# Kernel optimization log

Measured on AMD Instinct MI355X. Metric: run time of the kernel, lower is better.

Reference implementation:

```python
import jax, jax.numpy as jnp
import numpy as np

H_GRID, W_GRID = 32, 32
KH, KW = 7, 11
NUM_HEADS = 8


def local_window_mask(H, W, kh, kw):
    # Token (h,w) may attend to (h',w') iff |h-h'|<=kh//2 and |w-w'|<=kw//2
    # (equivalent to the padded/cropped construction in the torch module).
    hh = jnp.arange(H)
    ww = jnp.arange(W)
    ok_h = jnp.abs(hh[:, None] - hh[None, :]) <= kh // 2  # [H,H]
    ok_w = jnp.abs(ww[:, None] - ww[None, :]) <= kw // 2  # [W,W]
    ok = ok_h[:, None, :, None] & ok_w[None, :, None, :]  # [H,W,H,W]
    ok = ok.reshape(H * W, H * W)
    return jnp.where(ok, 0.0, -jnp.inf)[None, None]  # [1,1,N,N]


def setup_inputs() -> dict:
    key = jax.random.key(0)
    k1, k2, k3, k4, k5 = jax.random.split(key, 5)
    B, N, E = 8, H_GRID * W_GRID, 256
    return {
        "x": jax.random.normal(k1, (B, N, E), dtype=jnp.float32),
        "qkv_w": jax.random.normal(k2, (3 * E, E), dtype=jnp.float32) * 0.02,
        "qkv_b": jax.random.normal(k3, (3 * E,), dtype=jnp.float32) * 0.02,
        "proj_w": jax.random.normal(k4, (E, E), dtype=jnp.float32) * 0.02,
        "proj_b": jax.random.normal(k5, (E,), dtype=jnp.float32) * 0.02,
    }


def reference(x, qkv_w, qkv_b, proj_w, proj_b):
    B, N, E = x.shape
    dh = E // NUM_HEADS
    scale = E ** (-0.5)  # note: embed_dim scaling, as in the original module
    qkv = x @ qkv_w.T + qkv_b                       # [B,N,3E]
    qkv = qkv.reshape(B, N, 3, NUM_HEADS, dh).transpose(2, 0, 3, 1, 4)
    q, k, v = qkv[0] * scale, qkv[1], qkv[2]        # [B,H,N,dh]
    attn = jnp.einsum('bhnd,bhmd->bhnm', q, k)      # [B,H,N,N]
    attn = attn + local_window_mask(H_GRID, W_GRID, KH, KW)
    attn = jax.nn.softmax(attn, axis=-1)
    out = jnp.einsum('bhnm,bhmd->bhnd', attn, v)    # [B,H,N,dh]
    out = out.transpose(0, 2, 1, 3).reshape(B, N, E)
    return out @ proj_w.T + proj_b
```

## Files before the change

kernel.cpp:

```cpp
#include <hip/hip_runtime.h>
#include <math.h>

constexpr int Bb = 8;
constexpr int Ns = 1024;
constexpr int Es = 256;
constexpr int NH = 8;
constexpr int DH = 32;
constexpr int Mrows = Bb * Ns;
constexpr int NX = Mrows * Es;
constexpr int NP = Es * Es;

typedef __bf16 bf16x8 __attribute__((ext_vector_type(8)));
typedef float  f32x4  __attribute__((ext_vector_type(4)));
union U4B8 { uint4 u; bf16x8 b; unsigned short s[8]; };

__device__ __forceinline__ unsigned short f2bf(float f) {
    union { float f; unsigned u; } c; c.f = f;
    unsigned r = (c.u + 0x7FFFu + ((c.u >> 16) & 1u)) >> 16;
    return (unsigned short)r;
}
__device__ __forceinline__ float bf2f(unsigned short h) {
    union { unsigned u; float f; } c; c.u = ((unsigned)h) << 16;
    return c.f;
}

#define GLD 72
#define PST 232

__global__ __launch_bounds__(256, 4)
void qkv_gemm(const float* __restrict__ x, const float* __restrict__ qkv_w,
              const float* __restrict__ qkv_b, const float* __restrict__ proj_w,
              unsigned short* __restrict__ qo, unsigned short* __restrict__ ko,
              unsigned short* __restrict__ vto, unsigned short* __restrict__ pwb)
{
    __shared__ unsigned short As[64 * GLD];
    __shared__ unsigned short Ws[64 * GLD];

    const int t = threadIdx.x;

    if (blockIdx.x >= 1536) {
        int i = ((int)(blockIdx.x - 1536) * 256 + t) * 4;
        float4 f = *(const float4*)(proj_w + i);
        ushort4 u;
        u.x = f2bf(f.x); u.y = f2bf(f.y); u.z = f2bf(f.z); u.w = f2bf(f.w);
        *(ushort4*)(pwb + i) = u;
        return;
    }

    const int m0 = (blockIdx.x & 127) * 64;
    const int j0 = (blockIdx.x >> 7) * 64;

    const int srow = t >> 2;
    const int scol = (t & 3) * 16;

    const int lane = t & 63;
    const int wave = t >> 6;
    const int wm = (wave & 1) * 32;
    const int wn = (wave >> 1) * 32;
    const int fm = lane & 15;
    const int fq = lane >> 4;

    f32x4 acc[2][2];
    #pragma unroll
    for (int i = 0; i < 2; i++)
        #pragma unroll
        for (int j = 0; j < 2; j++)
            acc[i][j] = (f32x4){0.f, 0.f, 0.f, 0.f};

    const float* Arow = x + (size_t)(m0 + srow) * Es;
    const float* Wrow = qkv_w + (size_t)(j0 + srow) * Es;

    for (int k0 = 0; k0 < Es; k0 += 64) {
        float4 av[4], wv[4];
        #pragma unroll
        for (int i = 0; i < 4; i++) {
            av[i] = *(const float4*)(Arow + k0 + scol + 4 * i);
            wv[i] = *(const float4*)(Wrow + k0 + scol + 4 * i);
        }
        U4B8 pa0, pa1, pw0, pw1;
        #pragma unroll
        for (int i = 0; i < 2; i++) {
            pa0.s[4*i+0] = f2bf(av[i].x);   pa0.s[4*i+1] = f2bf(av[i].y);
            pa0.s[4*i+2] = f2bf(av[i].z);   pa0.s[4*i+3] = f2bf(av[i].w);
            pa1.s[4*i+0] = f2bf(av[i+2].x); pa1.s[4*i+1] = f2bf(av[i+2].y);
            pa1.s[4*i+2] = f2bf(av[i+2].z); pa1.s[4*i+3] = f2bf(av[i+2].w);
            pw0.s[4*i+0] = f2bf(wv[i].x);   pw0.s[4*i+1] = f2bf(wv[i].y);
            pw0.s[4*i+2] = f2bf(wv[i].z);   pw0.s[4*i+3] = f2bf(wv[i].w);
            pw1.s[4*i+0] = f2bf(wv[i+2].x); pw1.s[4*i+1] = f2bf(wv[i+2].y);
            pw1.s[4*i+2] = f2bf(wv[i+2].z); pw1.s[4*i+3] = f2bf(wv[i+2].w);
        }
        __syncthreads();
        *(uint4*)&As[srow * GLD + scol]     = pa0.u;
        *(uint4*)&As[srow * GLD + scol + 8] = pa1.u;
        *(uint4*)&Ws[srow * GLD + scol]     = pw0.u;
        *(uint4*)&Ws[srow * GLD + scol + 8] = pw1.u;
        __syncthreads();
        #pragma unroll
        for (int ks = 0; ks < 64; ks += 32) {
            U4B8 af0, af1, bf0, bf1;
            af0.u = *(const uint4*)&As[(wm +      fm) * GLD + ks + fq * 8];
            af1.u = *(const uint4*)&As[(wm + 16 + fm) * GLD + ks + fq * 8];
            bf0.u = *(const uint4*)&Ws[(wn +      fm) * GLD + ks + fq * 8];
            bf1.u = *(const uint4*)&Ws[(wn + 16 + fm) * GLD + ks + fq * 8];
            acc[0][0] = __builtin_amdgcn_mfma_f32_16x16x32_bf16(af0.b, bf0.b, acc[0][0], 0, 0, 0);
            acc[0][1] = __builtin_amdgcn_mfma_f32_16x16x32_bf16(af0.b, bf1.b, acc[0][1], 0, 0, 0);
            acc[1][0] = __builtin_amdgcn_mfma_f32_16x16x32_bf16(af1.b, bf0.b, acc[1][0], 0, 0, 0);
            acc[1][1] = __builtin_amdgcn_mfma_f32_16x16x32_bf16(af1.b, bf1.b, acc[1][1], 0, 0, 0);
        }
    }

    #pragma unroll
    for (int mt = 0; mt < 2; mt++) {
        #pragma unroll
        for (int nt = 0; nt < 2; nt++) {
            #pragma unroll
            for (int r = 0; r < 4; r++) {
                int row = m0 + wm + mt * 16 + fq * 4 + r;
                int col = j0 + wn + nt * 16 + fm;
                float val = acc[mt][nt][r] + qkv_b[col];
                int part = col >> 8;
                int head = (col >> 5) & 7;
                int d = col & 31;
                int b = row >> 10;
                int n = row & 1023;
                int bh = b * NH + head;
                if (part == 0)
                    qo[((size_t)bh * Ns + n) * DH + d] = f2bf(val * 0.0625f);
                else if (part == 1)
                    ko[((size_t)bh * Ns + n) * DH + d] = f2bf(val);
                else
                    vto[((size_t)bh * DH + d) * Ns + n] = f2bf(val);
            }
        }
    }
}

__global__ __launch_bounds__(256)
void attn_mfma2(const unsigned short* __restrict__ qb, const unsigned short* __restrict__ kb,
                const unsigned short* __restrict__ vtb, unsigned short* __restrict__ aob)
{
    __shared__ unsigned short Pb[32 * PST];
    __shared__ float pmax[2][32];
    __shared__ float psum[2][32];

    const int blk = blockIdx.x;
    const int hq  = blk & 31;
    const int bh  = blk >> 5;
    const int t   = threadIdx.x;
    const int lane = t & 63;
    const int w    = t >> 6;
    const int fm = lane & 15;
    const int fq = lane >> 4;

    int n0c = (hq - 3) * 32;
    n0c = n0c < 0 ? 0 : (n0c > Ns - 224 ? Ns - 224 : n0c);

    const int qbase = (w & 1) * 16;
    const int sel   = w >> 1;
    const int dbase = (w >> 1) * 16;

    const unsigned short* vrow = vtb + ((size_t)bh * DH + dbase + fm) * Ns;
    uint4 vpre[7];
    #pragma unroll
    for (int i = 0; i < 7; i++)
        vpre[i] = *(const uint4*)(vrow + n0c + i * 32 + fq * 8);

    U4B8 qa;
    qa.u = *(const uint4*)(qb + ((size_t)bh * Ns + hq * 32 + qbase + fm) * DH + fq * 8);

    f32x4 sv[7];
    #pragma unroll
    for (int i = 0; i < 7; i++) {
        int kt = sel + 2 * i;
        U4B8 kf;
        kf.u = *(const uint4*)(kb + ((size_t)bh * Ns + n0c + kt * 16 + fm) * DH + fq * 8);
        sv[i] = __builtin_amdgcn_mfma_f32_16x16x32_bf16(qa.b, kf.b, (f32x4){0.f,0.f,0.f,0.f}, 0, 0, 0);
    }

    float mx[4] = {-INFINITY, -INFINITY, -INFINITY, -INFINITY};
    #pragma unroll
    for (int i = 0; i < 7; i++) {
        int g = n0c + (sel + 2 * i) * 16 + fm;
        int gh = g >> 5, gw = g & 31;
        int dhh = gh - hq;
        bool okh = (dhh >= -3) && (dhh <= 3);
        #pragma unroll
        for (int r = 0; r < 4; r++) {
            int qc = qbase + fq * 4 + r;
            int dww = gw - qc;
            bool ok = okh && (dww >= -5) && (dww <= 5);
            float s = ok ? sv[i][r] : -INFINITY;
            sv[i][r] = s;
            mx[r] = fmaxf(mx[r], s);
        }
    }
    #pragma unroll
    for (int r = 0; r < 4; r++)
        #pragma unroll
        for (int m = 1; m < 16; m <<= 1)
            mx[r] = fmaxf(mx[r], __shfl_xor(mx[r], m));
    if (fm == 0) {
        #pragma unroll
        for (int r = 0; r < 4; r++)
            pmax[sel][qbase + fq * 4 + r] = mx[r];
    }
    __syncthreads();

    float M[4];
    #pragma unroll
    for (int r = 0; r < 4; r++) {
        int qc = qbase + fq * 4 + r;
        M[r] = fmaxf(pmax[0][qc], pmax[1][qc]);
    }

    float sm[4] = {0.f, 0.f, 0.f, 0.f};
    #pragma unroll
    for (int i = 0; i < 7; i++) {
        int kt = sel + 2 * i;
        #pragma unroll
        for (int r = 0; r < 4; r++) {
            float p = __expf(sv[i][r] - M[r]);
            unsigned short pu = f2bf(p);
            Pb[(qbase + fq * 4 + r) * PST + kt * 16 + fm] = pu;
            sm[r] += bf2f(pu);
        }
    }
    #pragma unroll
    for (int r = 0; r < 4; r++)
        #pragma unroll
        for (int m = 1; m < 16; m <<= 1)
            sm[r] += __shfl_xor(sm[r], m);
    if (fm == 0) {
        #pragma unroll
        for (int r = 0; r < 4; r++)
            psum[sel][qbase + fq * 4 + r] = sm[r];
    }
    __syncthreads();

    f32x4 acc = (f32x4){0.f, 0.f, 0.f, 0.f};
    #pragma unroll
    for (int i = 0; i < 7; i++) {
        U4B8 pa, vb;
        pa.u = *(const uint4*)&Pb[(qbase + fm) * PST + i * 32 + fq * 8];
        vb.u = vpre[i];
        acc = __builtin_amdgcn_mfma_f32_16x16x32_bf16(pa.b, vb.b, acc, 0, 0, 0);
    }

    const int b = bh >> 3, h = bh & 7;
    #pragma unroll
    for (int r = 0; r < 4; r++) {
        int qq = qbase + fq * 4 + r;
        float inv = 1.f / (psum[0][qq] + psum[1][qq]);
        aob[((size_t)(b * Ns) + hq * 32 + qq) * Es + h * DH + dbase + fm] = f2bf(acc[r] * inv);
    }
}

__global__ __launch_bounds__(256, 4)
void proj_gemm(const unsigned short* __restrict__ A, const unsigned short* __restrict__ Wb,
               const float* __restrict__ bias, float* __restrict__ out)
{
    __shared__ unsigned short As[64 * GLD];
    __shared__ unsigned short Ws[64 * GLD];

    const int t = threadIdx.x;
    const int m0 = (blockIdx.x & 127) * 64;
    const int j0 = (blockIdx.x >> 7) * 64;

    const int srow = t >> 2;
    const int scol = (t & 3) * 16;

    const int lane = t & 63;
    const int wave = t >> 6;
    const int wm = (wave & 1) * 32;
    const int wn = (wave >> 1) * 32;
    const int fm = lane & 15;
    const int fq = lane >> 4;

    f32x4 acc[2][2];
    #pragma unroll
    for (int i = 0; i < 2; i++)
        #pragma unroll
        for (int j = 0; j < 2; j++)
            acc[i][j] = (f32x4){0.f, 0.f, 0.f, 0.f};

    const unsigned short* Arow = A + (size_t)(m0 + srow) * Es;
    const unsigned short* Wrow = Wb + (size_t)(j0 + srow) * Es;

    for (int k0 = 0; k0 < Es; k0 += 64) {
        uint4 a0 = *(const uint4*)(Arow + k0 + scol);
        uint4 a1 = *(const uint4*)(Arow + k0 + scol + 8);
        uint4 w0 = *(const uint4*)(Wrow + k0 + scol);
        uint4 w1 = *(const uint4*)(Wrow + k0 + scol + 8);
        __syncthreads();
        *(uint4*)&As[srow * GLD + scol]     = a0;
        *(uint4*)&As[srow * GLD + scol + 8] = a1;
        *(uint4*)&Ws[srow * GLD + scol]     = w0;
        *(uint4*)&Ws[srow * GLD + scol + 8] = w1;
        __syncthreads();
        #pragma unroll
        for (int ks = 0; ks < 64; ks += 32) {
            U4B8 af0, af1, bf0, bf1;
            af0.u = *(const uint4*)&As[(wm +      fm) * GLD + ks + fq * 8];
            af1.u = *(const uint4*)&As[(wm + 16 + fm) * GLD + ks + fq * 8];
            bf0.u = *(const uint4*)&Ws[(wn +      fm) * GLD + ks + fq * 8];
            bf1.u = *(const uint4*)&Ws[(wn + 16 + fm) * GLD + ks + fq * 8];
            acc[0][0] = __builtin_amdgcn_mfma_f32_16x16x32_bf16(af0.b, bf0.b, acc[0][0], 0, 0, 0);
            acc[0][1] = __builtin_amdgcn_mfma_f32_16x16x32_bf16(af0.b, bf1.b, acc[0][1], 0, 0, 0);
            acc[1][0] = __builtin_amdgcn_mfma_f32_16x16x32_bf16(af1.b, bf0.b, acc[1][0], 0, 0, 0);
            acc[1][1] = __builtin_amdgcn_mfma_f32_16x16x32_bf16(af1.b, bf1.b, acc[1][1], 0, 0, 0);
        }
    }

    #pragma unroll
    for (int mt = 0; mt < 2; mt++) {
        #pragma unroll
        for (int nt = 0; nt < 2; nt++) {
            #pragma unroll
            for (int r = 0; r < 4; r++) {
                int row = m0 + wm + mt * 16 + fq * 4 + r;
                int col = j0 + wn + nt * 16 + fm;
                out[(size_t)row * Es + col] = acc[mt][nt][r] + bias[col];
            }
        }
    }
}

extern "C" void kernel_launch(void* const* d_in, const int* in_sizes, int n_in,
                              void* d_out, int out_size, void* d_ws, size_t ws_size,
                              hipStream_t stream) {
    const float* x      = (const float*)d_in[0];
    const float* qkv_w  = (const float*)d_in[1];
    const float* qkv_b  = (const float*)d_in[2];
    const float* proj_w = (const float*)d_in[3];
    const float* proj_b = (const float*)d_in[4];
    float* out = (float*)d_out;

    unsigned short* qb  = (unsigned short*)d_ws;
    unsigned short* kb  = qb + NX;
    unsigned short* vtb = kb + NX;
    unsigned short* pwb = vtb + NX;
    unsigned short* aob = pwb + NP;

    qkv_gemm<<<dim3(1600), dim3(256), 0, stream>>>(
        x, qkv_w, qkv_b, proj_w, qb, kb, vtb, pwb);

    attn_mfma2<<<dim3(Bb * NH * 32), dim3(256), 0, stream>>>(qb, kb, vtb, aob);

    proj_gemm<<<dim3(Mrows / 64 * (Es / 64)), dim3(256), 0, stream>>>(
        aob, pwb, proj_b, out);
}
```

Before: 104.9 us.

## Pre-cast inputs and weights to bf16 in a separate kernel; remap attention block order

Adds a cast kernel that converts x, qkv_w and proj_w to bf16 once, so the QKV GEMM loads bf16 tiles directly instead of reloading fp32 and converting in every block (x was re-read by 12 column blocks). It also reorders the attention block index so the batch varies fastest, changing which (b,h,q-tile) blocks run concurrently and how they hit cache. The cost is an extra kernel launch and an extra write and read of a bf16 copy of x.

```diff
diff --git a/kernel.cpp b/kernel.cpp
--- a/kernel.cpp
+++ b/kernel.cpp
@@ -8,6 +8,7 @@
 constexpr int DH = 32;
 constexpr int Mrows = Bb * Ns;
 constexpr int NX = Mrows * Es;
+constexpr int NQ = 3 * Es * Es;
 constexpr int NP = Es * Es;
 
 typedef __bf16 bf16x8 __attribute__((ext_vector_type(8)));
@@ -27,26 +28,34 @@
 #define GLD 72
 #define PST 232
 
+__global__ __launch_bounds__(256)
+void cast_all(const float* __restrict__ x, const float* __restrict__ wq,
+              const float* __restrict__ wp, unsigned short* __restrict__ xb,
+              unsigned short* __restrict__ wqb, unsigned short* __restrict__ wpb)
+{
+    int i = (blockIdx.x * 256 + threadIdx.x) * 8;
+    const float* src; unsigned short* dst;
+    if (i < NX)            { src = x  + i;             dst = xb  + i; }
+    else if (i < NX + NQ)  { src = wq + (i - NX);      dst = wqb + (i - NX); }
+    else                   { src = wp + (i - NX - NQ); dst = wpb + (i - NX - NQ); }
+    float4 f0 = *(const float4*)src;
+    float4 f1 = *(const float4*)(src + 4);
+    U4B8 u;
+    u.s[0] = f2bf(f0.x); u.s[1] = f2bf(f0.y); u.s[2] = f2bf(f0.z); u.s[3] = f2bf(f0.w);
+    u.s[4] = f2bf(f1.x); u.s[5] = f2bf(f1.y); u.s[6] = f2bf(f1.z); u.s[7] = f2bf(f1.w);
+    *(uint4*)dst = u.u;
+}
+
 __global__ __launch_bounds__(256, 4)
-void qkv_gemm(const float* __restrict__ x, const float* __restrict__ qkv_w,
-              const float* __restrict__ qkv_b, const float* __restrict__ proj_w,
+void qkv_gemm(const unsigned short* __restrict__ A, const unsigned short* __restrict__ W,
+              const float* __restrict__ qkv_b,
               unsigned short* __restrict__ qo, unsigned short* __restrict__ ko,
-              unsigned short* __restrict__ vto, unsigned short* __restrict__ pwb)
+              unsigned short* __restrict__ vto)
 {
     __shared__ unsigned short As[64 * GLD];
     __shared__ unsigned short Ws[64 * GLD];
 
     const int t = threadIdx.x;
-
-    if (blockIdx.x >= 1536) {
-        int i = ((int)(blockIdx.x - 1536) * 256 + t) * 4;
-        float4 f = *(const float4*)(proj_w + i);
-        ushort4 u;
-        u.x = f2bf(f.x); u.y = f2bf(f.y); u.z = f2bf(f.z); u.w = f2bf(f.w);
-        *(ushort4*)(pwb + i) = u;
-        return;
-    }
-
     const int m0 = (blockIdx.x & 127) * 64;
     const int j0 = (blockIdx.x >> 7) * 64;
 
@@ -67,33 +76,19 @@
         for (int j = 0; j < 2; j++)
             acc[i][j] = (f32x4){0.f, 0.f, 0.f, 0.f};
 
-    const float* Arow = x + (size_t)(m0 + srow) * Es;
-    const float* Wrow = qkv_w + (size_t)(j0 + srow) * Es;
+    const unsigned short* Arow = A + (size_t)(m0 + srow) * Es;
+    const unsigned short* Wrow = W + (size_t)(j0 + srow) * Es;
 
     for (int k0 = 0; k0 < Es; k0 += 64) {
-        float4 av[4], wv[4];
-        #pragma unroll
-        for (int i = 0; i < 4; i++) {
-            av[i] = *(const float4*)(Arow + k0 + scol + 4 * i);
-            wv[i] = *(const float4*)(Wrow + k0 + scol + 4 * i);
-        }
-        U4B8 pa0, pa1, pw0, pw1;
-        #pragma unroll
-        for (int i = 0; i < 2; i++) {
-            pa0.s[4*i+0] = f2bf(av[i].x);   pa0.s[4*i+1] = f2bf(av[i].y);
-            pa0.s[4*i+2] = f2bf(av[i].z);   pa0.s[4*i+3] = f2bf(av[i].w);
-            pa1.s[4*i+0] = f2bf(av[i+2].x); pa1.s[4*i+1] = f2bf(av[i+2].y);
-            pa1.s[4*i+2] = f2bf(av[i+2].z); pa1.s[4*i+3] = f2bf(av[i+2].w);
-            pw0.s[4*i+0] = f2bf(wv[i].x);   pw0.s[4*i+1] = f2bf(wv[i].y);
-            pw0.s[4*i+2] = f2bf(wv[i].z);   pw0.s[4*i+3] = f2bf(wv[i].w);
-            pw1.s[4*i+0] = f2bf(wv[i+2].x); pw1.s[4*i+1] = f2bf(wv[i+2].y);
-            pw1.s[4*i+2] = f2bf(wv[i+2].z); pw1.s[4*i+3] = f2bf(wv[i+2].w);
-        }
+        uint4 a0 = *(const uint4*)(Arow + k0 + scol);
+        uint4 a1 = *(const uint4*)(Arow + k0 + scol + 8);
+        uint4 w0 = *(const uint4*)(Wrow + k0 + scol);
+        uint4 w1 = *(const uint4*)(Wrow + k0 + scol + 8);
         __syncthreads();
-        *(uint4*)&As[srow * GLD + scol]     = pa0.u;
-        *(uint4*)&As[srow * GLD + scol + 8] = pa1.u;
-        *(uint4*)&Ws[srow * GLD + scol]     = pw0.u;
-        *(uint4*)&Ws[srow * GLD + scol + 8] = pw1.u;
+        *(uint4*)&As[srow * GLD + scol]     = a0;
+        *(uint4*)&As[srow * GLD + scol + 8] = a1;
+        *(uint4*)&Ws[srow * GLD + scol]     = w0;
+        *(uint4*)&Ws[srow * GLD + scol + 8] = w1;
         __syncthreads();
         #pragma unroll
         for (int ks = 0; ks < 64; ks += 32) {
@@ -144,8 +139,12 @@
     __shared__ float psum[2][32];
 
     const int blk = blockIdx.x;
-    const int hq  = blk & 31;
-    const int bh  = blk >> 5;
+    const int b   = blk & 7;
+    const int u   = blk >> 3;
+    const int h   = u & 7;
+    const int hq  = u >> 3;
+    const int bh  = b * NH + h;
+
     const int t   = threadIdx.x;
     const int lane = t & 63;
     const int w    = t >> 6;
@@ -246,7 +245,6 @@
         acc = __builtin_amdgcn_mfma_f32_16x16x32_bf16(pa.b, vb.b, acc, 0, 0, 0);
     }
 
-    const int b = bh >> 3, h = bh & 7;
     #pragma unroll
     for (int r = 0; r < 4; r++) {
         int qq = qbase + fq * 4 + r;
@@ -335,14 +333,18 @@
     const float* proj_b = (const float*)d_in[4];
     float* out = (float*)d_out;
 
-    unsigned short* qb  = (unsigned short*)d_ws;
+    unsigned short* xb  = (unsigned short*)d_ws;
+    unsigned short* wqb = xb + NX;
+    unsigned short* pwb = wqb + NQ;
+    unsigned short* qb  = pwb + NP;
     unsigned short* kb  = qb + NX;
     unsigned short* vtb = kb + NX;
-    unsigned short* pwb = vtb + NX;
-    unsigned short* aob = pwb + NP;
-
-    qkv_gemm<<<dim3(1600), dim3(256), 0, stream>>>(
-        x, qkv_w, qkv_b, proj_w, qb, kb, vtb, pwb);
+    unsigned short* aob = vtb + NX;
+
+    cast_all<<<dim3((NX + NQ + NP) / 8 / 256), dim3(256), 0, stream>>>(
+        x, qkv_w, proj_w, xb, wqb, pwb);
+
+    qkv_gemm<<<dim3(1536), dim3(256), 0, stream>>>(xb, wqb, qkv_b, qb, kb, vtb);
 
     attn_mfma2<<<dim3(Bb * NH * 32), dim3(256), 0, stream>>>(qb, kb, vtb, aob);
 
```

Result: faster. 102.2 us (-2.5%).
